# Performance work log

Hardware: AMD Instinct MI355X
Metric: run time of the kernel (lower is better)

Reference implementation:

```python
import jax, jax.numpy as jnp
import numpy as np

K = 8        # num capsules
DD = 64      # per-capsule dim (delta_d)
D = K * DD   # 512
T = 16384    # num target nodes (segments)
NB = 100000  # num neighbor nodes
E = 131072   # num edges
ROUIT = 3
BETA = 0.5


def seg_softmax(p, seg, num):
    # softmax over entries sharing the same segment id (axis 0)
    m = jax.lax.stop_gradient(jax.ops.segment_max(p, seg, num_segments=num))
    e = jnp.exp(p - m[seg])
    s = jax.ops.segment_sum(e, seg, num_segments=num)
    return e / s[seg]


def l2norm(x):
    # F.normalize along last axis with eps=1e-12
    n = jnp.sqrt(jnp.sum(x * x, axis=-1, keepdims=True))
    return x / jnp.maximum(n, 1e-12)


def setup_inputs() -> dict:
    key = jax.random.key(0)
    ks = jax.random.split(key, 9)
    return {
        "x_nb": jax.random.normal(ks[0], (NB, 512), dtype=jnp.float32),
        "ppr": jax.random.uniform(ks[1], (E,), dtype=jnp.float32),
        "pca_w": jax.random.normal(ks[2], (512, D), dtype=jnp.float32) * 0.02,
        "pca_b": jnp.zeros((D,), dtype=jnp.float32),
        "mlp_w": jax.random.normal(ks[3], (D, 40), dtype=jnp.float32) * 0.02,
        "mlp_b": jnp.zeros((40,), dtype=jnp.float32),
        "row_idx": jnp.sort(jax.random.randint(ks[4], (E,), 0, T, dtype=jnp.int32)),
        "col_idx": jax.random.randint(ks[5], (E,), 0, NB, dtype=jnp.int32),
        "x_idx": jax.random.randint(ks[6], (T,), 0, NB, dtype=jnp.int32),
    }


def reference(x_nb, ppr, pca_w, pca_b, mlp_w, mlp_b, row_idx, col_idx, x_idx):
    # pca projection + relu
    x = jax.nn.relu(x_nb @ pca_w + pca_b)            # (NB, D)
    # segment softmax of ppr over targets
    ppr = seg_softmax(ppr, row_idx, T)               # (E,)
    # is_xNorm: per-capsule l2 normalization
    x = l2norm(x.reshape(-1, K, DD)).reshape(-1, D)
    z = x[col_idx]                                   # (E, D) gathered neighbors
    zk = z.reshape(-1, K, DD)                        # (E, K, DD)
    # init_mtd == 2: ppr-weighted scatter-sum init
    u = jax.ops.segment_sum(z * ppr[:, None], row_idx, num_segments=T)  # (T, D)
    for it in range(ROUIT):
        uk = u[row_idx].reshape(-1, K, DD)           # (E, K, DD)
        p = jnp.einsum('ekd,ekd->ek', uk, zk)        # (E, K) capsule logits
        # attention == 1: segment softmax then blend with ppr
        p = seg_softmax(p, row_idx, T)
        p = BETA * p + (1.0 - BETA) * ppr[:, None]
        # final segment softmax
        p = seg_softmax(p, row_idx, T)
        u = jax.ops.segment_sum(zk * p[:, :, None], row_idx, num_segments=T)  # (T, K, DD)
        if it < ROUIT - 1:
            u = l2norm(u)
        u = u.reshape(T, D)
    out = jax.nn.relu(u)                             # dropout is identity at eval
    logits = out @ mlp_w + mlp_b                     # (T, nclass)
    return jax.nn.log_softmax(logits, axis=1)
```

## Files before the change

kernel.cpp:

```cpp
#include <hip/hip_runtime.h>
#include <cstdint>
#include <cstddef>

#define NB_N 100000
#define E_N  131072
#define T_N  16384
#define D_N  512
#define NCLS 40
#define NTILES 782
#define CAPR 12

typedef unsigned short u16;
typedef unsigned int   u32;
typedef __attribute__((ext_vector_type(8))) short  short8;
typedef __attribute__((ext_vector_type(4))) float  floatx4;

__device__ __forceinline__ u16 f2bf(float f) {
  u32 u = __float_as_uint(f);
  return (u16)((u + 0x7fffu + ((u >> 16) & 1u)) >> 16);
}
__device__ __forceinline__ void unpack8(uint4 z, float* f) {
  f[0] = __uint_as_float(z.x << 16);
  f[1] = __uint_as_float(z.x & 0xffff0000u);
  f[2] = __uint_as_float(z.y << 16);
  f[3] = __uint_as_float(z.y & 0xffff0000u);
  f[4] = __uint_as_float(z.z << 16);
  f[5] = __uint_as_float(z.z & 0xffff0000u);
  f[6] = __uint_as_float(z.w << 16);
  f[7] = __uint_as_float(z.w & 0xffff0000u);
}
__device__ __forceinline__ void gload_lds16(const void* g, void* s) {
  __builtin_amdgcn_global_load_lds(
      (const __attribute__((address_space(1))) unsigned int*)g,
      (__attribute__((address_space(3))) unsigned int*)s, 16, 0, 0);
}
__device__ __forceinline__ u32 cvtpk_bf16(float lo, float hi) {
  u32 r;
  asm("v_cvt_pk_bf16_f32 %0, %1, %2" : "=v"(r) : "v"(lo), "v"(hi));
  return r;
}

__global__ void conv_bt(const float* __restrict__ w, u16* __restrict__ Bt) {
  int i = blockIdx.x * 256 + threadIdx.x;
  int n = i >> 9, k = i & 511;
  Bt[i] = f2bf(w[k * 512 + n]);
}

__global__ void conv_bt2(const float* __restrict__ w, u16* __restrict__ Bt2) {
  int i = blockIdx.x * 256 + threadIdx.x;
  int n = i >> 9, k = i & 511;
  Bt2[i] = (n < NCLS) ? f2bf(w[k * NCLS + n]) : (u16)0;
}

__global__ void build_offs(const int* __restrict__ rowi, int* __restrict__ offs) {
  int e = blockIdx.x * 256 + threadIdx.x;
  if (e >= E_N) return;
  int r  = rowi[e];
  int rp = (e == 0) ? -1 : rowi[e - 1];
  for (int t = rp + 1; t <= r; ++t) offs[t] = e;
  if (e == E_N - 1)
    for (int t = r + 1; t <= T_N; ++t) offs[t] = E_N;
}

__global__ void ppr_sm(const float* __restrict__ ppr, const int* __restrict__ offs,
                       float* __restrict__ pprn) {
  int t = blockIdx.x * 256 + threadIdx.x;
  int s = offs[t], en = offs[t + 1];
  if (s >= en) return;
  float m = -INFINITY;
  for (int e = s; e < en; ++e) m = fmaxf(m, ppr[e]);
  float sum = 0.f;
  for (int e = s; e < en; ++e) sum += expf(ppr[e] - m);
  float inv = 1.f / sum;
  for (int e = s; e < en; ++e) pprn[e] = expf(ppr[e] - m) * inv;
}

__global__ __launch_bounds__(256, 3) void gemm_pca(
    const float* __restrict__ A,
    const u16*   __restrict__ Bt,
    const float* __restrict__ bias,
    u16*         __restrict__ xn) {
  __shared__ u16 SMEM[24576];
  u16* As = SMEM;
  u16* Bs = SMEM + 8192;
  const int tid  = threadIdx.x;
  const int wid  = tid >> 6, lane = tid & 63;
  const int quad = lane >> 4, l16 = lane & 15;
  const int b  = blockIdx.x;
  const int mt = (b & 7) | ((b >> 5) << 3);
  if (mt >= NTILES) return;
  const int m0 = mt * 128;
  const int n0 = ((b >> 3) & 3) * 128;
  const int wm = (wid >> 1) * 64;
  const int wn = (wid & 1) * 64;
  const int sw = l16 & 7;

  floatx4 acc[4][4];
#pragma unroll
  for (int i = 0; i < 4; ++i)
#pragma unroll
    for (int j = 0; j < 4; ++j) acc[i][j] = (floatx4){0.f, 0.f, 0.f, 0.f};

  float4 pa0[4], pa1[4];

  auto issueA = [&](int k0) {
#pragma unroll
    for (int j = 0; j < 4; ++j) {
      int ci = j * 256 + tid;
      int row = ci >> 3, kc = ci & 7;
      int gm = m0 + row;
      if (gm > NB_N - 1) gm = NB_N - 1;
      const float* src = A + (size_t)gm * 512 + k0 + kc * 8;
      pa0[j] = *(const float4*)(src);
      pa1[j] = *(const float4*)(src + 4);
    }
  };
  auto writeA = [&]() {
#pragma unroll
    for (int j = 0; j < 4; ++j) {
      int ci = j * 256 + tid;
      int row = ci >> 3, kc = ci & 7;
      uint4 pk;
      pk.x = cvtpk_bf16(pa0[j].x, pa0[j].y);
      pk.y = cvtpk_bf16(pa0[j].z, pa0[j].w);
      pk.z = cvtpk_bf16(pa1[j].x, pa1[j].y);
      pk.w = cvtpk_bf16(pa1[j].z, pa1[j].w);
      int dc = kc ^ (row & 7);
      *(uint4*)(&As[(size_t)(row * 8 + dc) * 8]) = pk;
    }
  };
  auto issueB = [&](int k0, u16* dstB) {
#pragma unroll
    for (int j = 0; j < 4; ++j) {
      int ci  = j * 256 + wid * 64 + lane;
      int row = ci >> 3;
      int kcs = (lane & 7) ^ ((lane >> 3) & 7);
      gload_lds16(Bt + (size_t)(n0 + row) * 512 + k0 + kcs * 8,
                  &dstB[(size_t)(j * 256 + wid * 64) * 8]);
    }
  };

  issueA(0);
  issueB(0, Bs);
  issueB(64, Bs + 8192);
  writeA();
  issueA(64);
  asm volatile("s_waitcnt vmcnt(12) lgkmcnt(0)" ::: "memory");
  __builtin_amdgcn_s_barrier();
  __builtin_amdgcn_sched_barrier(0);

#pragma unroll
  for (int s = 0; s < 8; ++s) {
    const int cs = s & 1;
    const u16* Bsc = Bs + cs * 8192;
#pragma unroll
    for (int kk = 0; kk < 64; kk += 32) {
      short8 af[4], bf[4];
#pragma unroll
      for (int mi = 0; mi < 4; ++mi) {
        int c = (kk >> 3) + quad;
        af[mi] = *(const short8*)(&As[(wm + mi * 16 + l16) * 64 + ((c ^ sw) << 3)]);
      }
#pragma unroll
      for (int ni = 0; ni < 4; ++ni) {
        int c = (kk >> 3) + quad;
        bf[ni] = *(const short8*)(&Bsc[(wn + ni * 16 + l16) * 64 + ((c ^ sw) << 3)]);
      }
#pragma unroll
      for (int mi = 0; mi < 4; ++mi)
#pragma unroll
        for (int ni = 0; ni < 4; ++ni)
          acc[mi][ni] = __builtin_amdgcn_mfma_f32_16x16x32_bf16(af[mi], bf[ni],
                                                                acc[mi][ni], 0, 0, 0);
    }
    __builtin_amdgcn_s_barrier();
    __builtin_amdgcn_sched_barrier(0);
    if (s + 1 < 8) {
      if (s + 2 < 8) issueB((s + 2) * 64, Bs + cs * 8192);
      writeA();
      if (s + 2 < 8) {
        issueA((s + 2) * 64);
        asm volatile("s_waitcnt vmcnt(12) lgkmcnt(0)" ::: "memory");
      } else {
        asm volatile("s_waitcnt vmcnt(0) lgkmcnt(0)" ::: "memory");
      }
      __builtin_amdgcn_s_barrier();
      __builtin_amdgcn_sched_barrier(0);
    }
  }
  __syncthreads();

  u16* Os = SMEM;
#pragma unroll
  for (int mi = 0; mi < 4; ++mi) {
#pragma unroll
    for (int r = 0; r < 4; ++r) {
      int lrow = wm + mi * 16 + quad * 4 + r;
      float v[4];
      float ss = 0.f;
#pragma unroll
      for (int ni = 0; ni < 4; ++ni) {
        int n  = n0 + wn + ni * 16 + l16;
        float x = acc[mi][ni][r] + bias[n];
        x = fmaxf(x, 0.f);
        v[ni] = x;
        ss += x * x;
      }
      ss += __shfl_xor(ss, 1);
      ss += __shfl_xor(ss, 2);
      ss += __shfl_xor(ss, 4);
      ss += __shfl_xor(ss, 8);
      float sc = 1.f / fmaxf(sqrtf(ss), 1e-12f);
#pragma unroll
      for (int ni = 0; ni < 4; ++ni)
        Os[lrow * 128 + wn + ni * 16 + l16] = f2bf(v[ni] * sc);
    }
  }
  __syncthreads();
#pragma unroll
  for (int c8 = 0; c8 < 8; ++c8) {
    int idx = c8 * 256 + tid;
    int row = idx >> 4, chk = idx & 15;
    int gm = m0 + row;
    if (gm < NB_N) {
      uint4 val = *(const uint4*)(&Os[row * 128 + chk * 8]);
      *(uint4*)(xn + (size_t)gm * 512 + n0 + chk * 8) = val;
    }
  }
}

__device__ __forceinline__ void matvec16(const float (&g0)[16], const float (&g1)[16],
                                         float w0, float w1, int base,
                                         float& e0, float& e1) {
  e0 = 0.f; e1 = 0.f;
#pragma unroll
  for (int j = 0; j < 8; ++j) {
    float wj = __shfl(w0, base | j);
    e0 += g0[j] * wj;
    e1 += g1[j] * wj;
  }
#pragma unroll
  for (int j = 0; j < 8; ++j) {
    float wj = __shfl(w1, base | j);
    e0 += g0[8 + j] * wj;
    e1 += g1[8 + j] * wj;
  }
}

__device__ __forceinline__ void segsm2(float& d0, float& d1, bool v0, bool v1) {
  float m = fmaxf(v0 ? d0 : -INFINITY, v1 ? d1 : -INFINITY);
  m = fmaxf(m, __shfl_xor(m, 1));
  m = fmaxf(m, __shfl_xor(m, 2));
  m = fmaxf(m, __shfl_xor(m, 4));
  float e0 = v0 ? expf(d0 - m) : 0.f;
  float e1 = v1 ? expf(d1 - m) : 0.f;
  float s = e0 + e1;
  s += __shfl_xor(s, 1);
  s += __shfl_xor(s, 2);
  s += __shfl_xor(s, 4);
  float inv = 1.f / s;
  d0 = e0 * inv;
  d1 = e1 * inv;
}

__global__ __launch_bounds__(128, 4) void fused_all(
    const u16* __restrict__ xn, const int* __restrict__ coli,
    const int* __restrict__ offs, const float* __restrict__ pprn,
    u16* __restrict__ ub) {
  __shared__ __align__(16) float Glds[2][8 * 260];
  const int lane = threadIdx.x & 63;
  const int wv = threadIdx.x >> 6;
  const int t = blockIdx.x * 2 + wv;
  const int s = offs[t], en = offs[t + 1];
  int deg = en - s;
  if (deg > 64) deg = 64;

  int   mycol = (lane < deg) ? coli[s + lane] : 0;
  float myppr = (lane < deg) ? pprn[s + lane] : 0.f;

  float uf[8] = {0.f, 0.f, 0.f, 0.f, 0.f, 0.f, 0.f, 0.f};

  if (deg <= 16) {
    float* G = Glds[wv];
    const int esrc = lane & 15, kq = lane >> 4;
    int ce = __shfl(mycol, esrc);
    const u16* zb = xn + (size_t)ce * 512 + kq * 8;
    floatx4 gram[8];
#pragma unroll
    for (int c = 0; c < 8; ++c) {
      short8 f0 = *(const short8*)(zb + c * 64);
      short8 f1 = *(const short8*)(zb + c * 64 + 32);
      floatx4 gg = (floatx4){0.f, 0.f, 0.f, 0.f};
      gg = __builtin_amdgcn_mfma_f32_16x16x32_bf16(f0, f0, gg, 0, 0, 0);
      gg = __builtin_amdgcn_mfma_f32_16x16x32_bf16(f1, f1, gg, 0, 0, 0);
      gram[c] = gg;
    }
#pragma unroll
    for (int c = 0; c < 8; ++c)
      *(float4*)&G[c * 260 + esrc * 16 + kq * 4] = *(float4*)&gram[c];
    const int cc = lane >> 3, i0 = lane & 7;
    const int base = lane & 56;
    float g0[16], g1[16];
    {
      const float* r0 = &G[cc * 260 + i0 * 16];
      const float* r1 = &G[cc * 260 + (i0 + 8) * 16];
#pragma unroll
      for (int ch = 0; ch < 4; ++ch) {
        float4 a = *(const float4*)(r0 + ch * 4);
        float4 b = *(const float4*)(r1 + ch * 4);
        g0[ch * 4 + 0] = a.x; g0[ch * 4 + 1] = a.y;
        g0[ch * 4 + 2] = a.z; g0[ch * 4 + 3] = a.w;
        g1[ch * 4 + 0] = b.x; g1[ch * 4 + 1] = b.y;
        g1[ch * 4 + 2] = b.z; g1[ch * 4 + 3] = b.w;
      }
    }
    const bool v0 = i0 < deg, v1 = (i0 + 8) < deg;
    float pr0 = __shfl(myppr, i0);
    float pr1 = __shfl(myppr, i0 + 8);

    float d0, d1;
    matvec16(g0, g1, pr0, pr1, base, d0, d1);

    float w0 = 0.f, w1 = 0.f;
#pragma unroll
    for (int it = 0; it < 3; ++it) {
      segsm2(d0, d1, v0, v1);
      d0 = 0.5f * d0 + 0.5f * pr0;
      d1 = 0.5f * d1 + 0.5f * pr1;
      segsm2(d0, d1, v0, v1);
      w0 = d0; w1 = d1;
      if (it < 2) {
        float e0, e1;
        matvec16(g0, g1, w0, w1, base, e0, e1);
        float nv = w0 * e0 + w1 * e1;
        nv += __shfl_xor(nv, 1);
        nv += __shfl_xor(nv, 2);
        nv += __shfl_xor(nv, 4);
        float invn = 1.f / fmaxf(sqrtf(nv), 1e-12f);
        d0 = e0 * invn;
        d1 = e1 * invn;
      }
    }

#pragma unroll
    for (int j = 0; j < 16; ++j) {
      if (j < deg) {
        float wj = __shfl((j < 8) ? w0 : w1, base | (j & 7));
        int cj = __shfl(mycol, j);
        uint4 zz = *(const uint4*)(xn + (size_t)cj * 512 + lane * 8);
        float zf[8];
        unpack8(zz, zf);
#pragma unroll
        for (int q = 0; q < 8; ++q) uf[q] += wj * zf[q];
      }
    }
  } else {
    const int cap = lane >> 3;
    const int slot = lane >> 3;

    uint4 zreg[CAPR];
#pragma unroll
    for (int j = 0; j < CAPR; ++j) {
      if (j < deg) {
        int c = __shfl(mycol, j);
        zreg[j] = *(const uint4*)(xn + (size_t)c * 512 + lane * 8);
      }
    }

#pragma unroll
    for (int j = 0; j < CAPR; ++j) {
      if (j < deg) {
        float w = __shfl(myppr, j);
        float zf[8];
        unpack8(zreg[j], zf);
#pragma unroll
        for (int q = 0; q < 8; ++q) uf[q] += w * zf[q];
      }
    }
    for (int j = CAPR; j < deg; ++j) {
      float w = __shfl(myppr, j);
      int c = __shfl(mycol, j);
      uint4 zz = *(const uint4*)(xn + (size_t)c * 512 + lane * 8);
      float zf[8];
      unpack8(zz, zf);
#pragma unroll
      for (int q = 0; q < 8; ++q) uf[q] += w * zf[q];
    }

    float Preg[8];

    for (int it = 0; it < 3; ++it) {
#pragma unroll
      for (int j = 0; j < CAPR; ++j) {
        if (j < deg) {
          float zf[8];
          unpack8(zreg[j], zf);
          float d = uf[0]*zf[0] + uf[1]*zf[1] + uf[2]*zf[2] + uf[3]*zf[3] +
                    uf[4]*zf[4] + uf[5]*zf[5] + uf[6]*zf[6] + uf[7]*zf[7];
          d += __shfl_xor(d, 1);
          d += __shfl_xor(d, 2);
          d += __shfl_xor(d, 4);
          float dc = __shfl(d, (lane & 7) << 3);
          if (slot == (j & 7)) Preg[j >> 3] = dc;
        }
      }
      for (int j = CAPR; j < deg; ++j) {
        int c = __shfl(mycol, j);
        uint4 zz = *(const uint4*)(xn + (size_t)c * 512 + lane * 8);
        float zf[8];
        unpack8(zz, zf);
        float d = uf[0]*zf[0] + uf[1]*zf[1] + uf[2]*zf[2] + uf[3]*zf[3] +
                  uf[4]*zf[4] + uf[5]*zf[5] + uf[6]*zf[6] + uf[7]*zf[7];
        d += __shfl_xor(d, 1);
        d += __shfl_xor(d, 2);
        d += __shfl_xor(d, 4);
        float dc = __shfl(d, (lane & 7) << 3);
        if (slot == (j & 7)) {
          int hi = j >> 3;
          if      (hi == 1) Preg[1] = dc;
          else if (hi == 2) Preg[2] = dc;
          else if (hi == 3) Preg[3] = dc;
          else if (hi == 4) Preg[4] = dc;
          else if (hi == 5) Preg[5] = dc;
          else if (hi == 6) Preg[6] = dc;
          else if (hi == 7) Preg[7] = dc;
        }
      }

      {
        float m1 = -INFINITY;
#pragma unroll
        for (int i = 0; i < 8; ++i)
          m1 = (slot + 8*i < deg) ? fmaxf(m1, Preg[i]) : m1;
        m1 = fmaxf(m1, __shfl_xor(m1, 8));
        m1 = fmaxf(m1, __shfl_xor(m1, 16));
        m1 = fmaxf(m1, __shfl_xor(m1, 32));
        float s1 = 0.f;
#pragma unroll
        for (int i = 0; i < 8; ++i)
          s1 += (slot + 8*i < deg) ? expf(Preg[i] - m1) : 0.f;
        s1 += __shfl_xor(s1, 8);
        s1 += __shfl_xor(s1, 16);
        s1 += __shfl_xor(s1, 32);
        float inv1 = 1.f / s1;
        float m2 = -INFINITY;
#pragma unroll
        for (int i = 0; i < 8; ++i) {
          int j = slot + 8*i;
          if (j < deg) {
            float pj = __shfl(myppr, j);
            float v = 0.5f * expf(Preg[i] - m1) * inv1 + 0.5f * pj;
            Preg[i] = v;
            m2 = fmaxf(m2, v);
          }
        }
        m2 = fmaxf(m2, __shfl_xor(m2, 8));
        m2 = fmaxf(m2, __shfl_xor(m2, 16));
        m2 = fmaxf(m2, __shfl_xor(m2, 32));
        float s2 = 0.f;
#pragma unroll
        for (int i = 0; i < 8; ++i)
          s2 += (slot + 8*i < deg) ? expf(Preg[i] - m2) : 0.f;
        s2 += __shfl_xor(s2, 8);
        s2 += __shfl_xor(s2, 16);
        s2 += __shfl_xor(s2, 32);
        float inv2 = 1.f / s2;
#pragma unroll
        for (int i = 0; i < 8; ++i)
          if (slot + 8*i < deg) Preg[i] = expf(Preg[i] - m2) * inv2;
      }

      float acc[8] = {0.f, 0.f, 0.f, 0.f, 0.f, 0.f, 0.f, 0.f};
#pragma unroll
      for (int j = 0; j < CAPR; ++j) {
        if (j < deg) {
          float w = __shfl(Preg[j >> 3], ((j & 7) << 3) | cap);
          float zf[8];
          unpack8(zreg[j], zf);
#pragma unroll
          for (int q = 0; q < 8; ++q) acc[q] += w * zf[q];
        }
      }
      for (int j = CAPR; j < deg; ++j) {
        int hi = j >> 3;
        float pr = Preg[1];
        if      (hi == 2) pr = Preg[2];
        else if (hi == 3) pr = Preg[3];
        else if (hi == 4) pr = Preg[4];
        else if (hi == 5) pr = Preg[5];
        else if (hi == 6) pr = Preg[6];
        else if (hi == 7) pr = Preg[7];
        float w = __shfl(pr, ((j & 7) << 3) | cap);
        int c = __shfl(mycol, j);
        uint4 zz = *(const uint4*)(xn + (size_t)c * 512 + lane * 8);
        float zf[8];
        unpack8(zz, zf);
#pragma unroll
        for (int q = 0; q < 8; ++q) acc[q] += w * zf[q];
      }
      if (it < 2) {
        float ss = 0.f;
#pragma unroll
        for (int q = 0; q < 8; ++q) ss += acc[q] * acc[q];
        ss += __shfl_xor(ss, 1);
        ss += __shfl_xor(ss, 2);
        ss += __shfl_xor(ss, 4);
        float sc = 1.f / fmaxf(sqrtf(ss), 1e-12f);
#pragma unroll
        for (int q = 0; q < 8; ++q) acc[q] *= sc;
      }
#pragma unroll
      for (int q = 0; q < 8; ++q) uf[q] = acc[q];
    }
  }

  uint4 pk;
  pk.x = (u32)f2bf(fmaxf(uf[0], 0.f)) | ((u32)f2bf(fmaxf(uf[1], 0.f)) << 16);
  pk.y = (u32)f2bf(fmaxf(uf[2], 0.f)) | ((u32)f2bf(fmaxf(uf[3], 0.f)) << 16);
  pk.z = (u32)f2bf(fmaxf(uf[4], 0.f)) | ((u32)f2bf(fmaxf(uf[5], 0.f)) << 16);
  pk.w = (u32)f2bf(fmaxf(uf[6], 0.f)) | ((u32)f2bf(fmaxf(uf[7], 0.f)) << 16);
  *(uint4*)(ub + (size_t)t * 512 + lane * 8) = pk;
}

__global__ __launch_bounds__(256) void mlp_gemm(
    const u16* __restrict__ ub, const u16* __restrict__ Bt2,
    const float* __restrict__ mb, float* __restrict__ out) {
  const int wid = threadIdx.x >> 6, lane = threadIdx.x & 63;
  const int quad = lane >> 4, l16 = lane & 15;
  const int m0 = blockIdx.x * 64 + wid * 16;

  floatx4 acc[4];
#pragma unroll
  for (int ni = 0; ni < 4; ++ni) acc[ni] = (floatx4){0.f, 0.f, 0.f, 0.f};

#pragma unroll 4
  for (int kk = 0; kk < 512; kk += 32) {
    short8 af = *(const short8*)(ub + (size_t)(m0 + l16) * 512 + kk + quad * 8);
#pragma unroll
    for (int ni = 0; ni < 4; ++ni) {
      short8 bf = *(const short8*)(Bt2 + (size_t)(ni * 16 + l16) * 512 + kk + quad * 8);
      acc[ni] = __builtin_amdgcn_mfma_f32_16x16x32_bf16(af, bf, acc[ni], 0, 0, 0);
    }
  }

#pragma unroll
  for (int r = 0; r < 4; ++r) {
    int t = m0 + quad * 4 + r;
    float v[4];
    float mx = -INFINITY;
#pragma unroll
    for (int ni = 0; ni < 4; ++ni) {
      int c = ni * 16 + l16;
      float lg = (c < NCLS) ? (acc[ni][r] + mb[c]) : -INFINITY;
      v[ni] = lg;
      mx = fmaxf(mx, lg);
    }
    mx = fmaxf(mx, __shfl_xor(mx, 1));
    mx = fmaxf(mx, __shfl_xor(mx, 2));
    mx = fmaxf(mx, __shfl_xor(mx, 4));
    mx = fmaxf(mx, __shfl_xor(mx, 8));
    float se = 0.f;
#pragma unroll
    for (int ni = 0; ni < 4; ++ni) {
      int c = ni * 16 + l16;
      if (c < NCLS) se += expf(v[ni] - mx);
    }
    se += __shfl_xor(se, 1);
    se += __shfl_xor(se, 2);
    se += __shfl_xor(se, 4);
    se += __shfl_xor(se, 8);
    float lse = mx + logf(se);
#pragma unroll
    for (int ni = 0; ni < 4; ++ni) {
      int c = ni * 16 + l16;
      if (c < NCLS) out[(size_t)t * NCLS + c] = v[ni] - lse;
    }
  }
}

extern "C" void kernel_launch(void* const* d_in, const int* in_sizes, int n_in,
                              void* d_out, int out_size, void* d_ws, size_t ws_size,
                              hipStream_t stream) {
  const float* x_nb  = (const float*)d_in[0];
  const float* ppr   = (const float*)d_in[1];
  const float* pca_w = (const float*)d_in[2];
  const float* pca_b = (const float*)d_in[3];
  const float* mlp_w = (const float*)d_in[4];
  const float* mlp_b = (const float*)d_in[5];
  const int* row_idx = (const int*)d_in[6];
  const int* col_idx = (const int*)d_in[7];
  float* out = (float*)d_out;

  char* ws = (char*)d_ws;
  const size_t OFF_BT   = 0;
  const size_t OFF_BT2  = 512 * 1024;
  const size_t OFF_PPRN = 640 * 1024;
  const size_t OFF_OFFS = 1152 * 1024;
  const size_t OFF_XN   = 1280 * 1024;
  const size_t OFF_UB   = OFF_XN + (size_t)NB_N * 512 * 2;
  u16*   Bt   = (u16*)(ws + OFF_BT);
  u16*   Bt2  = (u16*)(ws + OFF_BT2);
  float* pprn = (float*)(ws + OFF_PPRN);
  int*   offs = (int*)(ws + OFF_OFFS);
  u16*   xn   = (u16*)(ws + OFF_XN);
  u16*   ub   = (u16*)(ws + OFF_UB);

  conv_bt<<<1024, 256, 0, stream>>>(pca_w, Bt);
  conv_bt2<<<128, 256, 0, stream>>>(mlp_w, Bt2);
  build_offs<<<512, 256, 0, stream>>>(row_idx, offs);
  ppr_sm<<<64, 256, 0, stream>>>(ppr, offs, pprn);

  gemm_pca<<<98 * 32, 256, 0, stream>>>(x_nb, Bt, pca_b, xn);

  fused_all<<<T_N / 2, 128, 0, stream>>>(xn, col_idx, offs, pprn, ub);

  mlp_gemm<<<256, 256, 0, stream>>>(ub, Bt2, mlp_b, out);
}
```

Baseline: 450.8 us.

## Merge prep kernels, tile weight transpose, and compute ppr softmax in fused kernel

Three small setup kernels (weight transpose, MLP weight conversion, segment offset build) are merged into a single launch, and the PCA weight transpose now goes through a shared-memory tile so reads and writes are both coalesced. The separate per-segment ppr softmax kernel is removed; the softmax is instead computed with wavefront shuffles inside the fused routing kernel, using the raw ppr values. This cuts launch overhead and a serialized, poorly parallel kernel. The trade-off is that degree is capped at 64, so segments with more edges than that would be normalized differently, though the existing code already caps degree there.

```diff
diff --git a/kernel.cpp b/kernel.cpp
--- a/kernel.cpp
+++ b/kernel.cpp
@@ -40,39 +40,40 @@
   return r;
 }
 
-__global__ void conv_bt(const float* __restrict__ w, u16* __restrict__ Bt) {
-  int i = blockIdx.x * 256 + threadIdx.x;
-  int n = i >> 9, k = i & 511;
-  Bt[i] = f2bf(w[k * 512 + n]);
-}
-
-__global__ void conv_bt2(const float* __restrict__ w, u16* __restrict__ Bt2) {
-  int i = blockIdx.x * 256 + threadIdx.x;
-  int n = i >> 9, k = i & 511;
-  Bt2[i] = (n < NCLS) ? f2bf(w[k * NCLS + n]) : (u16)0;
-}
-
-__global__ void build_offs(const int* __restrict__ rowi, int* __restrict__ offs) {
-  int e = blockIdx.x * 256 + threadIdx.x;
-  if (e >= E_N) return;
-  int r  = rowi[e];
-  int rp = (e == 0) ? -1 : rowi[e - 1];
-  for (int t = rp + 1; t <= r; ++t) offs[t] = e;
-  if (e == E_N - 1)
-    for (int t = r + 1; t <= T_N; ++t) offs[t] = E_N;
-}
-
-__global__ void ppr_sm(const float* __restrict__ ppr, const int* __restrict__ offs,
-                       float* __restrict__ pprn) {
-  int t = blockIdx.x * 256 + threadIdx.x;
-  int s = offs[t], en = offs[t + 1];
-  if (s >= en) return;
-  float m = -INFINITY;
-  for (int e = s; e < en; ++e) m = fmaxf(m, ppr[e]);
-  float sum = 0.f;
-  for (int e = s; e < en; ++e) sum += expf(ppr[e] - m);
-  float inv = 1.f / sum;
-  for (int e = s; e < en; ++e) pprn[e] = expf(ppr[e] - m) * inv;
+__global__ void prep(const float* __restrict__ w, const float* __restrict__ w2,
+                     const int* __restrict__ rowi,
+                     u16* __restrict__ Bt, u16* __restrict__ Bt2,
+                     int* __restrict__ offs) {
+  const int b = blockIdx.x, tid = threadIdx.x;
+  if (b < 64) {
+    __shared__ float T[64][65];
+    const int tr = b >> 3, tc = b & 7;
+    const int c0 = tid & 63;
+    const int r0 = tid >> 6;
+#pragma unroll
+    for (int i = 0; i < 16; ++i) {
+      int kl = r0 * 16 + i;
+      T[kl][c0] = w[(size_t)(tr * 64 + kl) * 512 + tc * 64 + c0];
+    }
+    __syncthreads();
+#pragma unroll
+    for (int i = 0; i < 16; ++i) {
+      int nl = r0 + i * 4;
+      Bt[(size_t)(tc * 64 + nl) * 512 + tr * 64 + c0] = f2bf(T[c0][nl]);
+    }
+  } else if (b < 192) {
+    int i = (b - 64) * 256 + tid;
+    int n = i >> 9, k = i & 511;
+    Bt2[i] = (n < NCLS) ? f2bf(w2[k * NCLS + n]) : (u16)0;
+  } else {
+    int e = (b - 192) * 256 + tid;
+    if (e >= E_N) return;
+    int r  = rowi[e];
+    int rp = (e == 0) ? -1 : rowi[e - 1];
+    for (int t = rp + 1; t <= r; ++t) offs[t] = e;
+    if (e == E_N - 1)
+      for (int t = r + 1; t <= T_N; ++t) offs[t] = E_N;
+  }
 }
 
 __global__ __launch_bounds__(256, 3) void gemm_pca(
@@ -265,7 +266,7 @@
 
 __global__ __launch_bounds__(128, 4) void fused_all(
     const u16* __restrict__ xn, const int* __restrict__ coli,
-    const int* __restrict__ offs, const float* __restrict__ pprn,
+    const int* __restrict__ offs, const float* __restrict__ ppr,
     u16* __restrict__ ub) {
   __shared__ __align__(16) float Glds[2][8 * 260];
   const int lane = threadIdx.x & 63;
@@ -276,7 +277,28 @@
   if (deg > 64) deg = 64;
 
   int   mycol = (lane < deg) ? coli[s + lane] : 0;
-  float myppr = (lane < deg) ? pprn[s + lane] : 0.f;
+  float praw  = (lane < deg) ? ppr[s + lane] : 0.f;
+
+  float myppr;
+  {
+    float v = (lane < deg) ? praw : -INFINITY;
+    float m = v;
+    m = fmaxf(m, __shfl_xor(m, 1));
+    m = fmaxf(m, __shfl_xor(m, 2));
+    m = fmaxf(m, __shfl_xor(m, 4));
+    m = fmaxf(m, __shfl_xor(m, 8));
+    m = fmaxf(m, __shfl_xor(m, 16));
+    m = fmaxf(m, __shfl_xor(m, 32));
+    float e = (lane < deg) ? expf(praw - m) : 0.f;
+    float ss = e;
+    ss += __shfl_xor(ss, 1);
+    ss += __shfl_xor(ss, 2);
+    ss += __shfl_xor(ss, 4);
+    ss += __shfl_xor(ss, 8);
+    ss += __shfl_xor(ss, 16);
+    ss += __shfl_xor(ss, 32);
+    myppr = e / ss;
+  }
 
   float uf[8] = {0.f, 0.f, 0.f, 0.f, 0.f, 0.f, 0.f, 0.f};
 
@@ -594,25 +616,20 @@
   char* ws = (char*)d_ws;
   const size_t OFF_BT   = 0;
   const size_t OFF_BT2  = 512 * 1024;
-  const size_t OFF_PPRN = 640 * 1024;
-  const size_t OFF_OFFS = 1152 * 1024;
-  const size_t OFF_XN   = 1280 * 1024;
+  const size_t OFF_OFFS = 640 * 1024;
+  const size_t OFF_XN   = 768 * 1024;
   const size_t OFF_UB   = OFF_XN + (size_t)NB_N * 512 * 2;
   u16*   Bt   = (u16*)(ws + OFF_BT);
   u16*   Bt2  = (u16*)(ws + OFF_BT2);
-  float* pprn = (float*)(ws + OFF_PPRN);
   int*   offs = (int*)(ws + OFF_OFFS);
   u16*   xn   = (u16*)(ws + OFF_XN);
   u16*   ub   = (u16*)(ws + OFF_UB);
 
-  conv_bt<<<1024, 256, 0, stream>>>(pca_w, Bt);
-  conv_bt2<<<128, 256, 0, stream>>>(mlp_w, Bt2);
-  build_offs<<<512, 256, 0, stream>>>(row_idx, offs);
-  ppr_sm<<<64, 256, 0, stream>>>(ppr, offs, pprn);
+  prep<<<704, 256, 0, stream>>>(pca_w, mlp_w, row_idx, Bt, Bt2, offs);
 
   gemm_pca<<<98 * 32, 256, 0, stream>>>(x_nb, Bt, pca_b, xn);
 
-  fused_all<<<T_N / 2, 128, 0, stream>>>(xn, col_idx, offs, pprn, ub);
+  fused_all<<<T_N / 2, 128, 0, stream>>>(xn, col_idx, offs, ppr, ub);
 
   mlp_gemm<<<256, 256, 0, stream>>>(ub, Bt2, mlp_b, out);
 }
```

Result: no change. 444.2 us (-1.5%).
